# Kernel tuning notes

Hardware: AMD Instinct MI355X
Metric: run time of the kernel (lower is better)

Reference implementation:

```python
import jax, jax.numpy as jnp
import numpy as np

M, TX, N_A, N_VALUES = 4096, 128, 512, 256
W_SCALE = 0.05  # keep gates in non-saturated range through 128 recurrent steps


def setup_inputs() -> dict:
    key = jax.random.key(0)
    ks = jax.random.split(key, 4)
    X = jax.random.normal(ks[0], (M, TX, N_VALUES), dtype=jnp.float32)
    a0 = jnp.zeros((M, N_A), dtype=jnp.float32)
    c0 = jnp.zeros((M, N_A), dtype=jnp.float32)
    # PyTorch LSTM params, gate order (i, f, g, o) stacked along dim 0
    W_ih = jax.random.normal(ks[1], (4 * N_A, N_VALUES), dtype=jnp.float32) * W_SCALE
    W_hh = jax.random.normal(ks[2], (4 * N_A, N_A), dtype=jnp.float32) * W_SCALE
    b_ih = jnp.zeros((4 * N_A,), dtype=jnp.float32)
    b_hh = jnp.zeros((4 * N_A,), dtype=jnp.float32)
    W_out = jax.random.normal(ks[3], (N_VALUES, N_A), dtype=jnp.float32) * W_SCALE
    b_out = jnp.zeros((N_VALUES,), dtype=jnp.float32)
    return {"X": X, "a0": a0, "c0": c0, "W_ih": W_ih, "W_hh": W_hh,
            "b_ih": b_ih, "b_hh": b_hh, "W_out": W_out, "b_out": b_out}


def reference(X, a0, c0, W_ih, W_hh, b_ih, b_hh, W_out, b_out):
    # One LSTM cell step + Linear projection per timestep (PyTorch gate order i,f,g,o).
    b = b_ih + b_hh

    def step(carry, x_t):
        h, c = carry
        gates = x_t @ W_ih.T + h @ W_hh.T + b  # [m, 4*n_a]
        i, f, g, o = jnp.split(gates, 4, axis=-1)
        c_new = jax.nn.sigmoid(f) * c + jax.nn.sigmoid(i) * jnp.tanh(g)
        h_new = jax.nn.sigmoid(o) * jnp.tanh(c_new)
        out = h_new @ W_out.T + b_out  # [m, n_values]
        return (h_new, c_new), out

    xs = jnp.swapaxes(X, 0, 1)  # [Tx, m, n_values] for scan over time
    (_, _), outs = jax.lax.scan(step, (a0, c0), xs)
    return outs  # [Tx, m, n_values] == stacked list of per-step outputs
```

## Files before the change

### kernel.cpp

```cpp
#include <hip/hip_runtime.h>
#include <math.h>

typedef _Float16 f16;
typedef _Float16 f16x8 __attribute__((ext_vector_type(8)));
typedef float f32x4 __attribute__((ext_vector_type(4)));
typedef unsigned int u32;
typedef unsigned short u16;

#define M_DIM 4096
#define T_X   128
#define NV    256
#define NA    512
#define NG    2048
#define NKT   24

__device__ __forceinline__ float sigf(float x) { return 1.0f / (1.0f + __expf(-x)); }
__device__ __forceinline__ float tanh_fast(float x) {
    float t = __expf(2.0f * x);
    return (t - 1.0f) / (t + 1.0f);
}

#define GLOAD_LDS16(G, L) \
    __builtin_amdgcn_global_load_lds((const __attribute__((address_space(1))) u32*)(G), \
                                     (__attribute__((address_space(3))) u32*)(L), 16, 0, 0)

__global__ void prep(const float* __restrict__ X,
                     const float* __restrict__ a0, const float* __restrict__ c0,
                     const float* __restrict__ W_ih, const float* __restrict__ W_hh,
                     const float* __restrict__ b_ih, const float* __restrict__ b_hh,
                     const float* __restrict__ W_out,
                     u16* __restrict__ Ha, float* __restrict__ c,
                     u16* __restrict__ BG, u16* __restrict__ BOs, u16* __restrict__ BOo,
                     float* __restrict__ bs, u16* __restrict__ Xf0)
{
    const int N_BG  = NKT * 16 * 4096;
    const int N_BOS = 16 * 16 * 512;
    const int N_BOO = 16 * 4 * 2048;
    const int N_BS  = NG;
    const int N_H   = 32 * 16 * 4096;
    const int N_XF  = 32 * 8 * 4096;
    const int N_C   = M_DIM * NA;
    const int NT = N_BG + N_BOS + N_BOO + N_BS + N_H + N_XF + N_C;
    for (int idx = blockIdx.x * blockDim.x + threadIdx.x; idx < NT;
         idx += gridDim.x * blockDim.x) {
        int i = idx;
        if (i < N_BG) {
            int tile = i >> 12, w = i & 4095;
            int jb = tile & 15, kt = tile >> 4;
            int f = w >> 9, lane = (w >> 3) & 63, e = w & 7;
            int wcc = f >> 2, g = f & 3;
            int n = g * NA + jb * 32 + wcc * 16 + (lane & 15);
            int k = kt * 32 + ((lane >> 4) << 3) + e;
            float v = (k < NV) ? W_ih[n * NV + k] : W_hh[n * NA + (k - NV)];
            BG[i] = __builtin_bit_cast(u16, (f16)v);
            continue;
        }
        i -= N_BG;
        if (i < N_BOS) {
            int tile = i >> 9, w = i & 511;
            int s = tile & 15, kt = tile >> 4;
            int lane = w >> 3, e = w & 7;
            int n = s * 16 + (lane & 15);
            int k = kt * 32 + ((lane >> 4) << 3) + e;
            BOs[i] = __builtin_bit_cast(u16, (f16)W_out[n * NA + k]);
            continue;
        }
        i -= N_BOS;
        if (i < N_BOO) {
            int tile = i >> 11, w = i & 2047;
            int nb = tile & 3, kt = tile >> 2;
            int f = w >> 9, lane = (w >> 3) & 63, e = w & 7;
            int n = nb * 64 + f * 16 + (lane & 15);
            int k = kt * 32 + ((lane >> 4) << 3) + e;
            BOo[i] = __builtin_bit_cast(u16, (f16)W_out[n * NA + k]);
            continue;
        }
        i -= N_BOO;
        if (i < N_BS) { bs[i] = b_ih[i] + b_hh[i]; continue; }
        i -= N_BS;
        if (i < N_H) {
            int tile = i >> 12, w = i & 4095;
            int kt = tile & 15, mb = tile >> 4;
            int mf = w >> 9, lane = (w >> 3) & 63, e = w & 7;
            int m = mb * 128 + mf * 16 + (lane & 15);
            int k = kt * 32 + ((lane >> 4) << 3) + e;
            Ha[i] = __builtin_bit_cast(u16, (f16)a0[m * NA + k]);
            continue;
        }
        i -= N_H;
        if (i < N_XF) {
            int tile = i >> 12, w = i & 4095;
            int kt = tile & 7, mb = tile >> 3;
            int mf = w >> 9, lane = (w >> 3) & 63, e = w & 7;
            int m = mb * 128 + mf * 16 + (lane & 15);
            int k = kt * 32 + ((lane >> 4) << 3) + e;
            Xf0[i] = __builtin_bit_cast(u16, (f16)X[(size_t)m * (T_X * NV) + k]);
            continue;
        }
        i -= N_XF;
        c[i] = c0[i];
    }
}

__global__ __launch_bounds__(256)
void step_fused(const float* __restrict__ X,
                const u16* __restrict__ Xf_cur, u16* __restrict__ Xf_next,
                const u16* __restrict__ Hin, u16* __restrict__ Hout,
                float* __restrict__ c,
                const u16* __restrict__ BG, const u16* __restrict__ BOs,
                const float* __restrict__ bs, const float* __restrict__ b_out,
                float* __restrict__ out_prev, int t, int do_out, int do_xconv)
{
    __shared__ char smem[65536];
    char* BO_lds = smem + 49152;

    const int id  = blockIdx.x;
    const int xcd = id & 7, g2 = id >> 3;
    const int jb  = g2 & 15;
    const int mb  = xcd + 8 * (g2 >> 4);

    const int tid = threadIdx.x, lane = tid & 63, wv = tid >> 6;
    const int wr = wv >> 1, wc = wv & 1;

    f32x4 acc[4][4];
    #pragma unroll
    for (int a = 0; a < 4; ++a)
        #pragma unroll
        for (int b = 0; b < 4; ++b) acc[a][b] = (f32x4){0.f, 0.f, 0.f, 0.f};
    f32x4 acc_o[4];
    #pragma unroll
    for (int a = 0; a < 4; ++a) acc_o[a] = (f32x4){0.f, 0.f, 0.f, 0.f};

    auto stage = [&](int ktn, int buf) {
        char* base = smem + buf * 16384;
        const char* asrc = (ktn < 8)
            ? (const char*)(Xf_cur + ((size_t)(mb * 8 + ktn)) * 4096)
            : (const char*)(Hin + ((size_t)(mb * 16 + (ktn - 8))) * 4096);
        GLOAD_LDS16(asrc + wv * 2048 + lane * 16,        base + wv * 2048);
        GLOAD_LDS16(asrc + wv * 2048 + 1024 + lane * 16, base + wv * 2048 + 1024);
        const char* bsrc = (const char*)(BG + ((size_t)(ktn * 16 + jb)) * 4096);
        GLOAD_LDS16(bsrc + wv * 2048 + lane * 16,        base + 8192 + wv * 2048);
        GLOAD_LDS16(bsrc + wv * 2048 + 1024 + lane * 16, base + 8192 + wv * 2048 + 1024);
    };
    auto compute = [&](int ktn, int buf) {
        const char* base = smem + buf * 16384;
        f16x8 af[4], bfr[4];
        #pragma unroll
        for (int g = 0; g < 4; ++g)
            bfr[g] = *(const f16x8*)(base + 8192 + (((wc * 4 + g) * 64 + lane) << 4));
        #pragma unroll
        for (int fm = 0; fm < 4; ++fm)
            af[fm] = *(const f16x8*)(base + (((wr * 4 + fm) * 64 + lane) << 4));
        #pragma unroll
        for (int fm = 0; fm < 4; ++fm)
            #pragma unroll
            for (int g = 0; g < 4; ++g)
                acc[fm][g] = __builtin_amdgcn_mfma_f32_16x16x32_f16(af[fm], bfr[g], acc[fm][g], 0, 0, 0);
        if (do_out && ktn >= 8 && ((ktn - 8) & 1) == wc) {
            f16x8 bo = *(const f16x8*)(BO_lds + (ktn - 8) * 1024 + lane * 16);
            #pragma unroll
            for (int fm = 0; fm < 4; ++fm)
                acc_o[fm] = __builtin_amdgcn_mfma_f32_16x16x32_f16(af[fm], bo, acc_o[fm], 0, 0, 0);
        }
    };

    #pragma unroll
    for (int i = 0; i < 4; ++i) {
        int kt = wv * 4 + i;
        const char* src = (const char*)(BOs + ((size_t)(kt * 16 + jb)) * 512);
        GLOAD_LDS16(src + lane * 16, BO_lds + kt * 1024);
    }
    stage(0, 0);
    stage(1, 1);

    int cur = 0;
    for (int kt = 0; kt < NKT - 1; ++kt) {
        asm volatile("s_waitcnt vmcnt(4)" ::: "memory");
        __builtin_amdgcn_s_barrier();
        if (kt + 2 < NKT) {
            int stb = cur + 2; if (stb >= 3) stb -= 3;
            stage(kt + 2, stb);
        }
        compute(kt, cur);
        ++cur; if (cur == 3) cur = 0;
    }
    asm volatile("s_waitcnt vmcnt(0)" ::: "memory");
    __builtin_amdgcn_s_barrier();
    compute(NKT - 1, cur);

    const int ll = lane & 15, lh = lane >> 4;
    const int colg = jb * 32 + wc * 16 + ll;
    float bsv[4];
    #pragma unroll
    for (int g = 0; g < 4; ++g) bsv[g] = bs[g * NA + colg];

    u16* htile = Hout + ((size_t)(mb * 16 + jb)) * 4096;
    const int ksub = wc * 2 + (ll >> 3);
    const int e = ll & 7;

    #pragma unroll
    for (int fm = 0; fm < 4; ++fm) {
        const int mf = wr * 4 + fm;
        #pragma unroll
        for (int q = 0; q < 4; ++q) {
            const int rloc = mf * 16 + lh * 4 + q;
            const size_t m = (size_t)mb * 128 + rloc;
            float gi = acc[fm][0][q] + bsv[0];
            float gf = acc[fm][1][q] + bsv[1];
            float gg = acc[fm][2][q] + bsv[2];
            float go = acc[fm][3][q] + bsv[3];
            float cv = c[m * NA + colg];
            float iv = sigf(gi), fv = sigf(gf);
            float gv = tanh_fast(gg), ov = sigf(go);
            float cn = fv * cv + iv * gv;
            float hn = ov * tanh_fast(cn);
            c[m * NA + colg] = cn;
            const int lanep = (lh * 4 + q) + 16 * ksub;
            htile[(mf * 64 + lanep) * 8 + e] = __builtin_bit_cast(u16, (f16)hn);
        }
    }

    if (do_out) {
        if (wc == 1) {
            float* P = (float*)(smem + wr * 4096);
            #pragma unroll
            for (int fm = 0; fm < 4; ++fm)
                #pragma unroll
                for (int q = 0; q < 4; ++q)
                    P[(fm * 16 + lh * 4 + q) * 16 + ll] = acc_o[fm][q];
        }
        __syncthreads();
        if (wc == 0) {
            const float* P = (const float*)(smem + wr * 4096);
            const float bo = b_out[jb * 16 + ll];
            #pragma unroll
            for (int fm = 0; fm < 4; ++fm)
                #pragma unroll
                for (int q = 0; q < 4; ++q) {
                    const int rloc = wr * 64 + fm * 16 + lh * 4 + q;
                    float v = acc_o[fm][q] + P[(fm * 16 + lh * 4 + q) * 16 + ll] + bo;
                    out_prev[((size_t)mb * 128 + rloc) * NV + jb * 16 + ll] = v;
                }
        }
    }

    if (do_xconv && jb < 8) {
        const int r = tid >> 1, kh = tid & 1;
        const float* xsrc = X + ((size_t)(mb * 128 + r) * T_X + (t + 1)) * NV + jb * 32 + kh * 16;
        f32x4 xv[4];
        #pragma unroll
        for (int i = 0; i < 4; ++i) xv[i] = *(const f32x4*)(xsrc + i * 4);
        u16* xt = Xf_next + ((size_t)(mb * 8 + jb)) * 4096;
        const int mf = r >> 4;
        #pragma unroll
        for (int s = 0; s < 2; ++s) {
            f16x8 v;
            #pragma unroll
            for (int j = 0; j < 8; ++j) v[j] = (f16)xv[s * 2 + (j >> 2)][j & 3];
            const int lanep = (r & 15) + 16 * (kh * 2 + s);
            *(f16x8*)(xt + (mf * 64 + lanep) * 8) = v;
        }
    }
}

__global__ __launch_bounds__(256)
void out_proj(const u16* __restrict__ Hin, const u16* __restrict__ BO,
              const float* __restrict__ b_out, float* __restrict__ out)
{
    __shared__ char smem[24576];

    const int id  = blockIdx.x;
    const int xcd = id & 7, g2 = id >> 3;
    const int nb  = g2 & 3;
    const int mb  = xcd + 8 * (g2 >> 2);

    const int tid = threadIdx.x, lane = tid & 63, wv = tid >> 6;
    const int wr = wv >> 1, wc = wv & 1;

    f32x4 acc[4][2];
    #pragma unroll
    for (int a = 0; a < 4; ++a) { acc[a][0] = (f32x4){0,0,0,0}; acc[a][1] = (f32x4){0,0,0,0}; }

    auto stage = [&](int kt, int buf) {
        char* base = smem + buf * 12288;
        const char* asrc = (const char*)(Hin + ((size_t)(mb * 16 + kt)) * 4096);
        GLOAD_LDS16(asrc + wv * 2048 + lane * 16,        base + wv * 2048);
        GLOAD_LDS16(asrc + wv * 2048 + 1024 + lane * 16, base + wv * 2048 + 1024);
        const char* bsrc = (const char*)(BO + ((size_t)(kt * 4 + nb)) * 2048);
        GLOAD_LDS16(bsrc + wv * 1024 + lane * 16, base + 8192 + wv * 1024);
    };
    auto compute = [&](int buf) {
        const char* base = smem + buf * 12288;
        f16x8 bfr[2];
        #pragma unroll
        for (int fq = 0; fq < 2; ++fq)
            bfr[fq] = *(const f16x8*)(base + 8192 + (((wc * 2 + fq) * 64 + lane) << 4));
        #pragma unroll
        for (int fm = 0; fm < 4; ++fm) {
            f16x8 af = *(const f16x8*)(base + (((wr * 4 + fm) * 64 + lane) << 4));
            #pragma unroll
            for (int fq = 0; fq < 2; ++fq)
                acc[fm][fq] = __builtin_amdgcn_mfma_f32_16x16x32_f16(af, bfr[fq], acc[fm][fq], 0, 0, 0);
        }
    };

    stage(0, 0);
    __syncthreads();
    for (int kt = 0; kt < 16; ++kt) {
        const int cur = kt & 1;
        if (kt + 1 < 16) stage(kt + 1, cur ^ 1);
        compute(cur);
        __syncthreads();
    }

    const int ll = lane & 15, lh = lane >> 4;
    float bov[2];
    #pragma unroll
    for (int fq = 0; fq < 2; ++fq) bov[fq] = b_out[nb * 64 + (wc * 2 + fq) * 16 + ll];

    #pragma unroll
    for (int fm = 0; fm < 4; ++fm)
        #pragma unroll
        for (int fq = 0; fq < 2; ++fq)
            #pragma unroll
            for (int q = 0; q < 4; ++q) {
                const int row = mb * 128 + wr * 64 + fm * 16 + lh * 4 + q;
                const int col = nb * 64 + (wc * 2 + fq) * 16 + ll;
                out[(size_t)row * NV + col] = acc[fm][fq][q] + bov[fq];
            }
}

extern "C" void kernel_launch(void* const* d_in, const int* in_sizes, int n_in,
                              void* d_out, int out_size, void* d_ws, size_t ws_size,
                              hipStream_t stream) {
    const float* X     = (const float*)d_in[0];
    const float* a0    = (const float*)d_in[1];
    const float* c0    = (const float*)d_in[2];
    const float* W_ih  = (const float*)d_in[3];
    const float* W_hh  = (const float*)d_in[4];
    const float* b_ih  = (const float*)d_in[5];
    const float* b_hh  = (const float*)d_in[6];
    const float* W_out = (const float*)d_in[7];
    const float* b_out = (const float*)d_in[8];
    float* out = (float*)d_out;

    char* w = (char*)d_ws;
    u16*   Ha   = (u16*)(w);
    u16*   Hb   = (u16*)(w + ((size_t)4 << 20));
    float* cbf  = (float*)(w + ((size_t)8 << 20));
    u16*   BG   = (u16*)(w + ((size_t)16 << 20));
    u16*   BOs  = (u16*)(w + ((size_t)19 << 20));
    u16*   BOo  = (u16*)(w + ((size_t)19 << 20) + 262144);
    float* bsv  = (float*)(w + ((size_t)19 << 20) + 524288);
    u16*   Xfa  = (u16*)(w + ((size_t)20 << 20));
    u16*   Xfb  = (u16*)(w + ((size_t)22 << 20));

    prep<<<8192, 256, 0, stream>>>(X, a0, c0, W_ih, W_hh, b_ih, b_hh, W_out,
                                   Ha, cbf, BG, BOs, BOo, bsv, Xfa);

    for (int t = 0; t < T_X; ++t) {
        const u16* hi = (t & 1) ? Hb : Ha;
        u16*       ho = (t & 1) ? Ha : Hb;
        const u16* xc = (t & 1) ? Xfb : Xfa;
        u16*       xn = (t & 1) ? Xfa : Xfb;
        float* outp = out + (size_t)(t > 0 ? t - 1 : 0) * M_DIM * NV;
        step_fused<<<512, 256, 0, stream>>>(X, xc, xn, hi, ho, cbf, BG, BOs, bsv, b_out,
                                            outp, t, t > 0 ? 1 : 0, t < T_X - 1 ? 1 : 0);
    }
    out_proj<<<128, 256, 0, stream>>>(Ha, BOo, b_out, out + (size_t)(T_X - 1) * M_DIM * NV);
}
```

Measured before the change: 3.539 ms.

## Replace per-timestep launches with a persistent cooperative kernel using grid sync

Replaces the 128 per-timestep kernel launches plus the final projection launch with one cooperative persistent kernel that loops over time and uses grid.sync between steps. The cell state now stays in registers across steps instead of round-tripping through global memory, and the output-projection weights and biases are loaded into LDS and registers once. This removes launch overhead and the per-step reloads, at the cost of a grid-wide barrier each step and needing all 512 blocks co-resident (2 per CU via launch bounds). The old multi-launch path remains as a fallback if the cooperative launch fails.

```diff
diff --git a/kernel.cpp b/kernel.cpp
--- a/kernel.cpp
+++ b/kernel.cpp
@@ -1,5 +1,8 @@
 #include <hip/hip_runtime.h>
+#include <hip/hip_cooperative_groups.h>
 #include <math.h>
+
+namespace cg = cooperative_groups;
 
 typedef _Float16 f16;
 typedef _Float16 f16x8 __attribute__((ext_vector_type(8)));
@@ -102,6 +105,234 @@
     }
 }
 
+__global__ __launch_bounds__(256, 2)
+void lstm_persistent(const float* __restrict__ X,
+                     u16* __restrict__ Xfa, u16* __restrict__ Xfb,
+                     u16* __restrict__ Ha, u16* __restrict__ Hb,
+                     const float* __restrict__ c0,
+                     const u16* __restrict__ BG, const u16* __restrict__ BOs,
+                     const float* __restrict__ bs, const float* __restrict__ b_out,
+                     float* __restrict__ out)
+{
+    __shared__ char smem[65536];
+    char* BO_lds = smem + 49152;
+    cg::grid_group grid = cg::this_grid();
+
+    const int id  = blockIdx.x;
+    const int xcd = id & 7, g2 = id >> 3;
+    const int jb  = g2 & 15;
+    const int mb  = xcd + 8 * (g2 >> 4);
+
+    const int tid = threadIdx.x, lane = tid & 63, wv = tid >> 6;
+    const int wr = wv >> 1, wc = wv & 1;
+    const int ll = lane & 15, lh = lane >> 4;
+    const int colg = jb * 32 + wc * 16 + ll;
+
+    #pragma unroll
+    for (int i = 0; i < 4; ++i) {
+        int kt = wv * 4 + i;
+        const char* src = (const char*)(BOs + ((size_t)(kt * 16 + jb)) * 512);
+        GLOAD_LDS16(src + lane * 16, BO_lds + kt * 1024);
+    }
+    float bsv[4];
+    #pragma unroll
+    for (int g = 0; g < 4; ++g) bsv[g] = bs[g * NA + colg];
+    float bo_r = b_out[jb * 16 + ll];
+    float cv[4][4];
+    #pragma unroll
+    for (int fm = 0; fm < 4; ++fm)
+        #pragma unroll
+        for (int q = 0; q < 4; ++q) {
+            const size_t m = (size_t)mb * 128 + (wr * 4 + fm) * 16 + lh * 4 + q;
+            cv[fm][q] = c0[m * NA + colg];
+        }
+    asm volatile("s_waitcnt vmcnt(0)" ::: "memory");
+    #pragma unroll
+    for (int g = 0; g < 4; ++g) asm volatile("" : "+v"(bsv[g]));
+    asm volatile("" : "+v"(bo_r));
+    #pragma unroll
+    for (int fm = 0; fm < 4; ++fm)
+        #pragma unroll
+        for (int q = 0; q < 4; ++q) asm volatile("" : "+v"(cv[fm][q]));
+    __syncthreads();
+
+    const u16* Xf_cur; u16* Xf_next;
+    const u16* Hin;    u16* Hout;
+
+    auto stage = [&](int ktn, int buf) {
+        char* base = smem + buf * 16384;
+        const char* asrc = (ktn < 8)
+            ? (const char*)(Xf_cur + ((size_t)(mb * 8 + ktn)) * 4096)
+            : (const char*)(Hin + ((size_t)(mb * 16 + (ktn - 8))) * 4096);
+        GLOAD_LDS16(asrc + wv * 2048 + lane * 16,        base + wv * 2048);
+        GLOAD_LDS16(asrc + wv * 2048 + 1024 + lane * 16, base + wv * 2048 + 1024);
+        const char* bsrc = (const char*)(BG + ((size_t)(ktn * 16 + jb)) * 4096);
+        GLOAD_LDS16(bsrc + wv * 2048 + lane * 16,        base + 8192 + wv * 2048);
+        GLOAD_LDS16(bsrc + wv * 2048 + 1024 + lane * 16, base + 8192 + wv * 2048 + 1024);
+    };
+    auto stageA = [&](int ktn, int buf) {
+        char* base = smem + buf * 16384;
+        const char* asrc = (const char*)(Hin + ((size_t)(mb * 16 + ktn)) * 4096);
+        GLOAD_LDS16(asrc + wv * 2048 + lane * 16,        base + wv * 2048);
+        GLOAD_LDS16(asrc + wv * 2048 + 1024 + lane * 16, base + wv * 2048 + 1024);
+    };
+
+    f32x4 acc[4][4];
+    f32x4 acc_o[4];
+
+    auto compute = [&](int ktn, int buf, int do_out) {
+        const char* base = smem + buf * 16384;
+        f16x8 af[4], bfr[4];
+        #pragma unroll
+        for (int g = 0; g < 4; ++g)
+            bfr[g] = *(const f16x8*)(base + 8192 + (((wc * 4 + g) * 64 + lane) << 4));
+        #pragma unroll
+        for (int fm = 0; fm < 4; ++fm)
+            af[fm] = *(const f16x8*)(base + (((wr * 4 + fm) * 64 + lane) << 4));
+        #pragma unroll
+        for (int fm = 0; fm < 4; ++fm)
+            #pragma unroll
+            for (int g = 0; g < 4; ++g)
+                acc[fm][g] = __builtin_amdgcn_mfma_f32_16x16x32_f16(af[fm], bfr[g], acc[fm][g], 0, 0, 0);
+        if (do_out && ktn >= 8 && ((ktn - 8) & 1) == wc) {
+            f16x8 bo = *(const f16x8*)(BO_lds + (ktn - 8) * 1024 + lane * 16);
+            #pragma unroll
+            for (int fm = 0; fm < 4; ++fm)
+                acc_o[fm] = __builtin_amdgcn_mfma_f32_16x16x32_f16(af[fm], bo, acc_o[fm], 0, 0, 0);
+        }
+    };
+    auto computeO = [&](int ktn, int buf) {
+        const char* base = smem + buf * 16384;
+        if ((ktn & 1) == wc) {
+            f16x8 bo = *(const f16x8*)(BO_lds + ktn * 1024 + lane * 16);
+            #pragma unroll
+            for (int fm = 0; fm < 4; ++fm) {
+                f16x8 af = *(const f16x8*)(base + (((wr * 4 + fm) * 64 + lane) << 4));
+                acc_o[fm] = __builtin_amdgcn_mfma_f32_16x16x32_f16(af, bo, acc_o[fm], 0, 0, 0);
+            }
+        }
+    };
+    auto reduce_out = [&](float* out_prev) {
+        if (wc == 1) {
+            float* P = (float*)(smem + wr * 4096);
+            #pragma unroll
+            for (int fm = 0; fm < 4; ++fm)
+                #pragma unroll
+                for (int q = 0; q < 4; ++q)
+                    P[(fm * 16 + lh * 4 + q) * 16 + ll] = acc_o[fm][q];
+        }
+        __syncthreads();
+        if (wc == 0) {
+            const float* P = (const float*)(smem + wr * 4096);
+            #pragma unroll
+            for (int fm = 0; fm < 4; ++fm)
+                #pragma unroll
+                for (int q = 0; q < 4; ++q) {
+                    const int rloc = wr * 64 + fm * 16 + lh * 4 + q;
+                    float v = acc_o[fm][q] + P[(fm * 16 + lh * 4 + q) * 16 + ll] + bo_r;
+                    out_prev[((size_t)mb * 128 + rloc) * NV + jb * 16 + ll] = v;
+                }
+        }
+    };
+
+    for (int t = 0; t < T_X; ++t) {
+        Xf_cur  = (t & 1) ? Xfb : Xfa;
+        Xf_next = (t & 1) ? Xfa : Xfb;
+        Hin     = (t & 1) ? Hb : Ha;
+        Hout    = (t & 1) ? Ha : Hb;
+        const int do_out = (t > 0);
+
+        #pragma unroll
+        for (int a = 0; a < 4; ++a) {
+            acc_o[a] = (f32x4){0.f, 0.f, 0.f, 0.f};
+            #pragma unroll
+            for (int b = 0; b < 4; ++b) acc[a][b] = (f32x4){0.f, 0.f, 0.f, 0.f};
+        }
+
+        stage(0, 0);
+        stage(1, 1);
+        int cur = 0;
+        for (int kt = 0; kt < NKT - 1; ++kt) {
+            asm volatile("s_waitcnt vmcnt(4)" ::: "memory");
+            __builtin_amdgcn_s_barrier();
+            if (kt + 2 < NKT) {
+                int stb = cur + 2; if (stb >= 3) stb -= 3;
+                stage(kt + 2, stb);
+            }
+            compute(kt, cur, do_out);
+            ++cur; if (cur == 3) cur = 0;
+        }
+        asm volatile("s_waitcnt vmcnt(0)" ::: "memory");
+        __builtin_amdgcn_s_barrier();
+        compute(NKT - 1, cur, do_out);
+
+        u16* htile = Hout + ((size_t)(mb * 16 + jb)) * 4096;
+        const int ksub = wc * 2 + (ll >> 3);
+        const int e = ll & 7;
+        #pragma unroll
+        for (int fm = 0; fm < 4; ++fm) {
+            const int mf = wr * 4 + fm;
+            #pragma unroll
+            for (int q = 0; q < 4; ++q) {
+                float gi = acc[fm][0][q] + bsv[0];
+                float gf = acc[fm][1][q] + bsv[1];
+                float gg = acc[fm][2][q] + bsv[2];
+                float go = acc[fm][3][q] + bsv[3];
+                float iv = sigf(gi), fv = sigf(gf);
+                float gv = tanh_fast(gg), ov = sigf(go);
+                float cn = fv * cv[fm][q] + iv * gv;
+                float hn = ov * tanh_fast(cn);
+                cv[fm][q] = cn;
+                const int lanep = (lh * 4 + q) + 16 * ksub;
+                htile[(mf * 64 + lanep) * 8 + e] = __builtin_bit_cast(u16, (f16)hn);
+            }
+        }
+
+        if (do_out) reduce_out(out + (size_t)(t - 1) * M_DIM * NV);
+
+        if (t < T_X - 1 && jb < 8) {
+            const int r = tid >> 1, kh = tid & 1;
+            const float* xsrc = X + ((size_t)(mb * 128 + r) * T_X + (t + 1)) * NV + jb * 32 + kh * 16;
+            f32x4 xv[4];
+            #pragma unroll
+            for (int i = 0; i < 4; ++i) xv[i] = *(const f32x4*)(xsrc + i * 4);
+            u16* xt = Xf_next + ((size_t)(mb * 8 + jb)) * 4096;
+            const int mf = r >> 4;
+            #pragma unroll
+            for (int s = 0; s < 2; ++s) {
+                f16x8 v;
+                #pragma unroll
+                for (int j = 0; j < 8; ++j) v[j] = (f16)xv[s * 2 + (j >> 2)][j & 3];
+                const int lanep = (r & 15) + 16 * (kh * 2 + s);
+                *(f16x8*)(xt + (mf * 64 + lanep) * 8) = v;
+            }
+        }
+
+        grid.sync();
+    }
+
+    Hin = Ha;
+    #pragma unroll
+    for (int a = 0; a < 4; ++a) acc_o[a] = (f32x4){0.f, 0.f, 0.f, 0.f};
+    stageA(0, 0);
+    stageA(1, 1);
+    int cur = 0;
+    for (int kt = 0; kt < 15; ++kt) {
+        asm volatile("s_waitcnt vmcnt(2)" ::: "memory");
+        __builtin_amdgcn_s_barrier();
+        if (kt + 2 < 16) {
+            int stb = cur + 2; if (stb >= 3) stb -= 3;
+            stageA(kt + 2, stb);
+        }
+        computeO(kt, cur);
+        ++cur; if (cur == 3) cur = 0;
+    }
+    asm volatile("s_waitcnt vmcnt(0)" ::: "memory");
+    __builtin_amdgcn_s_barrier();
+    computeO(15, cur);
+    reduce_out(out + (size_t)(T_X - 1) * M_DIM * NV);
+}
+
 __global__ __launch_bounds__(256)
 void step_fused(const float* __restrict__ X,
                 const u16* __restrict__ Xf_cur, u16* __restrict__ Xf_next,
@@ -209,10 +440,10 @@
             float gf = acc[fm][1][q] + bsv[1];
             float gg = acc[fm][2][q] + bsv[2];
             float go = acc[fm][3][q] + bsv[3];
-            float cv = c[m * NA + colg];
+            float cvv = c[m * NA + colg];
             float iv = sigf(gi), fv = sigf(gf);
             float gv = tanh_fast(gg), ov = sigf(go);
-            float cn = fv * cv + iv * gv;
+            float cn = fv * cvv + iv * gv;
             float hn = ov * tanh_fast(cn);
             c[m * NA + colg] = cn;
             const int lanep = (lh * 4 + q) + 16 * ksub;
@@ -358,14 +589,21 @@
     prep<<<8192, 256, 0, stream>>>(X, a0, c0, W_ih, W_hh, b_ih, b_hh, W_out,
                                    Ha, cbf, BG, BOs, BOo, bsv, Xfa);
 
-    for (int t = 0; t < T_X; ++t) {
-        const u16* hi = (t & 1) ? Hb : Ha;
-        u16*       ho = (t & 1) ? Ha : Hb;
-        const u16* xc = (t & 1) ? Xfb : Xfa;
-        u16*       xn = (t & 1) ? Xfa : Xfb;
-        float* outp = out + (size_t)(t > 0 ? t - 1 : 0) * M_DIM * NV;
-        step_fused<<<512, 256, 0, stream>>>(X, xc, xn, hi, ho, cbf, BG, BOs, bsv, b_out,
-                                            outp, t, t > 0 ? 1 : 0, t < T_X - 1 ? 1 : 0);
-    }
-    out_proj<<<128, 256, 0, stream>>>(Ha, BOo, b_out, out + (size_t)(T_X - 1) * M_DIM * NV);
+    void* args[] = {(void*)&X, (void*)&Xfa, (void*)&Xfb, (void*)&Ha, (void*)&Hb,
+                    (void*)&c0, (void*)&BG, (void*)&BOs, (void*)&bsv, (void*)&b_out,
+                    (void*)&out};
+    hipError_t err = hipLaunchCooperativeKernel((const void*)lstm_persistent,
+                                                dim3(512), dim3(256), args, 0, stream);
+    if (err != hipSuccess) {
+        for (int t = 0; t < T_X; ++t) {
+            const u16* hi = (t & 1) ? Hb : Ha;
+            u16*       ho = (t & 1) ? Ha : Hb;
+            const u16* xc = (t & 1) ? Xfb : Xfa;
+            u16*       xn = (t & 1) ? Xfa : Xfb;
+            float* outp = out + (size_t)(t > 0 ? t - 1 : 0) * M_DIM * NV;
+            step_fused<<<512, 256, 0, stream>>>(X, xc, xn, hi, ho, cbf, BG, BOs, bsv, b_out,
+                                                outp, t, t > 0 ? 1 : 0, t < T_X - 1 ? 1 : 0);
+        }
+        out_proj<<<128, 256, 0, stream>>>(Ha, BOo, b_out, out + (size_t)(T_X - 1) * M_DIM * NV);
+    }
 }
```

Result: slower. 10.20 ms (+188.1%).

## Prefetch cell state into registers and convert X two steps ahead with nontemporal I/O

Applied to the files above, without the earlier changes.

The cell state is stored in a per-thread contiguous layout, so each thread loads its 16 values as vector nontemporal loads at kernel start and writes them back after the gate math. This replaces the scattered per-element c reads and writes. X conversion moves to a triple buffer filled two steps ahead, and output and X accesses use nontemporal hints. Launch bounds now request two blocks per CU. The explicit vmcnt(0) wait at the start serializes the c load before the GEMM begins, which could hide less latency than intended.

```diff
diff --git a/kernel.cpp b/kernel.cpp
--- a/kernel.cpp
+++ b/kernel.cpp
@@ -29,16 +29,16 @@
                      const float* __restrict__ W_ih, const float* __restrict__ W_hh,
                      const float* __restrict__ b_ih, const float* __restrict__ b_hh,
                      const float* __restrict__ W_out,
-                     u16* __restrict__ Ha, float* __restrict__ c,
+                     u16* __restrict__ Ha, float* __restrict__ cws,
                      u16* __restrict__ BG, u16* __restrict__ BOs, u16* __restrict__ BOo,
-                     float* __restrict__ bs, u16* __restrict__ Xf0)
+                     float* __restrict__ bs, u16* __restrict__ Xf)
 {
     const int N_BG  = NKT * 16 * 4096;
     const int N_BOS = 16 * 16 * 512;
     const int N_BOO = 16 * 4 * 2048;
     const int N_BS  = NG;
     const int N_H   = 32 * 16 * 4096;
-    const int N_XF  = 32 * 8 * 4096;
+    const int N_XF  = 2 * 32 * 8 * 4096;
     const int N_C   = M_DIM * NA;
     const int NT = N_BG + N_BOS + N_BOO + N_BS + N_H + N_XF + N_C;
     for (int idx = blockIdx.x * blockDim.x + threadIdx.x; idx < NT;
@@ -89,24 +89,38 @@
         }
         i -= N_H;
         if (i < N_XF) {
-            int tile = i >> 12, w = i & 4095;
+            int b = i >> 20, j = i & 1048575;
+            int tile = j >> 12, w = j & 4095;
             int kt = tile & 7, mb = tile >> 3;
             int mf = w >> 9, lane = (w >> 3) & 63, e = w & 7;
             int m = mb * 128 + mf * 16 + (lane & 15);
             int k = kt * 32 + ((lane >> 4) << 3) + e;
-            Xf0[i] = __builtin_bit_cast(u16, (f16)X[(size_t)m * (T_X * NV) + k]);
+            Xf[i] = __builtin_bit_cast(u16, (f16)X[(size_t)m * (T_X * NV) + b * NV + k]);
             continue;
         }
         i -= N_XF;
-        c[i] = c0[i];
-    }
-}
-
-__global__ __launch_bounds__(256)
+        {
+            int id  = i >> 12;
+            int rem = i & 4095;
+            int tid = rem >> 4, r16 = rem & 15;
+            int fm = r16 >> 2, q = r16 & 3;
+            int xcd = id & 7, g2 = id >> 3;
+            int jb = g2 & 15, mb = xcd + 8 * (g2 >> 4);
+            int lane = tid & 63, wv = tid >> 6;
+            int wr = wv >> 1, wc = wv & 1;
+            int ll = lane & 15, lh = lane >> 4;
+            int m = mb * 128 + (wr * 4 + fm) * 16 + lh * 4 + q;
+            int col = jb * 32 + wc * 16 + ll;
+            cws[i] = c0[(size_t)m * NA + col];
+        }
+    }
+}
+
+__global__ __launch_bounds__(256, 2)
 void step_fused(const float* __restrict__ X,
-                const u16* __restrict__ Xf_cur, u16* __restrict__ Xf_next,
+                const u16* __restrict__ Xf_cur, u16* __restrict__ Xf_n2,
                 const u16* __restrict__ Hin, u16* __restrict__ Hout,
-                float* __restrict__ c,
+                float* __restrict__ cws,
                 const u16* __restrict__ BG, const u16* __restrict__ BOs,
                 const float* __restrict__ bs, const float* __restrict__ b_out,
                 float* __restrict__ out_prev, int t, int do_out, int do_xconv)
@@ -121,6 +135,14 @@
 
     const int tid = threadIdx.x, lane = tid & 63, wv = tid >> 6;
     const int wr = wv >> 1, wc = wv & 1;
+
+    f32x4 cv4[4];
+    {
+        const f32x4* cb = (const f32x4*)(cws + ((size_t)id * 256 + tid) * 16);
+        #pragma unroll
+        for (int i = 0; i < 4; ++i) cv4[i] = __builtin_nontemporal_load(cb + i);
+    }
+    asm volatile("s_waitcnt vmcnt(0)" ::: "memory");
 
     f32x4 acc[4][4];
     #pragma unroll
@@ -203,21 +225,23 @@
         const int mf = wr * 4 + fm;
         #pragma unroll
         for (int q = 0; q < 4; ++q) {
-            const int rloc = mf * 16 + lh * 4 + q;
-            const size_t m = (size_t)mb * 128 + rloc;
             float gi = acc[fm][0][q] + bsv[0];
             float gf = acc[fm][1][q] + bsv[1];
             float gg = acc[fm][2][q] + bsv[2];
             float go = acc[fm][3][q] + bsv[3];
-            float cv = c[m * NA + colg];
             float iv = sigf(gi), fv = sigf(gf);
             float gv = tanh_fast(gg), ov = sigf(go);
-            float cn = fv * cv + iv * gv;
+            float cn = fv * cv4[fm][q] + iv * gv;
             float hn = ov * tanh_fast(cn);
-            c[m * NA + colg] = cn;
+            cv4[fm][q] = cn;
             const int lanep = (lh * 4 + q) + 16 * ksub;
             htile[(mf * 64 + lanep) * 8 + e] = __builtin_bit_cast(u16, (f16)hn);
         }
+    }
+    {
+        f32x4* cb = (f32x4*)(cws + ((size_t)id * 256 + tid) * 16);
+        #pragma unroll
+        for (int i = 0; i < 4; ++i) __builtin_nontemporal_store(cv4[i], cb + i);
     }
 
     if (do_out) {
@@ -239,18 +263,20 @@
                 for (int q = 0; q < 4; ++q) {
                     const int rloc = wr * 64 + fm * 16 + lh * 4 + q;
                     float v = acc_o[fm][q] + P[(fm * 16 + lh * 4 + q) * 16 + ll] + bo;
-                    out_prev[((size_t)mb * 128 + rloc) * NV + jb * 16 + ll] = v;
+                    __builtin_nontemporal_store(
+                        v, out_prev + ((size_t)mb * 128 + rloc) * NV + jb * 16 + ll);
                 }
         }
     }
 
     if (do_xconv && jb < 8) {
         const int r = tid >> 1, kh = tid & 1;
-        const float* xsrc = X + ((size_t)(mb * 128 + r) * T_X + (t + 1)) * NV + jb * 32 + kh * 16;
+        const float* xsrc = X + ((size_t)(mb * 128 + r) * T_X + (t + 2)) * NV + jb * 32 + kh * 16;
         f32x4 xv[4];
         #pragma unroll
-        for (int i = 0; i < 4; ++i) xv[i] = *(const f32x4*)(xsrc + i * 4);
-        u16* xt = Xf_next + ((size_t)(mb * 8 + jb)) * 4096;
+        for (int i = 0; i < 4; ++i)
+            xv[i] = __builtin_nontemporal_load((const f32x4*)(xsrc + i * 4));
+        u16* xt = Xf_n2 + ((size_t)(mb * 8 + jb)) * 4096;
         const int mf = r >> 4;
         #pragma unroll
         for (int s = 0; s < 2; ++s) {
@@ -326,7 +352,8 @@
             for (int q = 0; q < 4; ++q) {
                 const int row = mb * 128 + wr * 64 + fm * 16 + lh * 4 + q;
                 const int col = nb * 64 + (wc * 2 + fq) * 16 + ll;
-                out[(size_t)row * NV + col] = acc[fm][fq][q] + bov[fq];
+                __builtin_nontemporal_store(acc[fm][fq][q] + bov[fq],
+                                            out + (size_t)row * NV + col);
             }
 }
 
@@ -347,25 +374,24 @@
     char* w = (char*)d_ws;
     u16*   Ha   = (u16*)(w);
     u16*   Hb   = (u16*)(w + ((size_t)4 << 20));
-    float* cbf  = (float*)(w + ((size_t)8 << 20));
+    float* cws  = (float*)(w + ((size_t)8 << 20));
     u16*   BG   = (u16*)(w + ((size_t)16 << 20));
     u16*   BOs  = (u16*)(w + ((size_t)19 << 20));
     u16*   BOo  = (u16*)(w + ((size_t)19 << 20) + 262144);
     float* bsv  = (float*)(w + ((size_t)19 << 20) + 524288);
-    u16*   Xfa  = (u16*)(w + ((size_t)20 << 20));
-    u16*   Xfb  = (u16*)(w + ((size_t)22 << 20));
+    u16*   Xf   = (u16*)(w + ((size_t)20 << 20));
 
     prep<<<8192, 256, 0, stream>>>(X, a0, c0, W_ih, W_hh, b_ih, b_hh, W_out,
-                                   Ha, cbf, BG, BOs, BOo, bsv, Xfa);
+                                   Ha, cws, BG, BOs, BOo, bsv, Xf);
 
     for (int t = 0; t < T_X; ++t) {
         const u16* hi = (t & 1) ? Hb : Ha;
         u16*       ho = (t & 1) ? Ha : Hb;
-        const u16* xc = (t & 1) ? Xfb : Xfa;
-        u16*       xn = (t & 1) ? Xfa : Xfb;
+        const u16* xc = Xf + (size_t)(t % 3) * 1048576;
+        u16*       xn = Xf + (size_t)((t + 2) % 3) * 1048576;
         float* outp = out + (size_t)(t > 0 ? t - 1 : 0) * M_DIM * NV;
-        step_fused<<<512, 256, 0, stream>>>(X, xc, xn, hi, ho, cbf, BG, BOs, bsv, b_out,
-                                            outp, t, t > 0 ? 1 : 0, t < T_X - 1 ? 1 : 0);
+        step_fused<<<512, 256, 0, stream>>>(X, xc, xn, hi, ho, cws, BG, BOs, bsv, b_out,
+                                            outp, t, t > 0 ? 1 : 0, t < T_X - 2 ? 1 : 0);
     }
     out_proj<<<128, 256, 0, stream>>>(Ha, BOo, b_out, out + (size_t)(T_X - 1) * M_DIM * NV);
 }
```

New measurement: 3.951 ms. +11.6%, slower.
